# Kernel tuning notes

Measured on AMD Instinct MI355X. Metric: run time of the kernel, lower is better.

Reference implementation:

```python
import jax, jax.numpy as jnp
import numpy as np
import math

B, S, D_IN, D_OUT = 2, 2048, 2048, 2048
N_HEADS, N_KV = 32, 8
HEAD_DIM = D_OUT // N_HEADS  # 64
GROUP = N_HEADS // N_KV      # 4


def _rope_tables(seq_len, head_dim, base=10000.0):
    inv_freq = 1.0 / (base ** (jnp.arange(0, head_dim, 2, dtype=jnp.float32) / head_dim))
    angles = jnp.arange(seq_len, dtype=jnp.float32)[:, None] * inv_freq[None, :]  # [S, hd/2]
    angles = jnp.concatenate([angles, angles], axis=-1)  # [S, hd]
    return jnp.cos(angles), jnp.sin(angles)


def setup_inputs() -> dict:
    key = jax.random.key(0)
    kx, kq, kk, kv, ko = jax.random.split(key, 5)
    x = jax.random.normal(kx, (B, S, D_IN), dtype=jnp.float32)
    # causal mask: True where attention is disallowed (j > i)
    mask = jnp.triu(jnp.ones((S, S), dtype=bool), k=1)
    cos, sin = _rope_tables(S, HEAD_DIM)
    scale = 0.02
    Wq = jax.random.normal(kq, (D_IN, D_OUT), dtype=jnp.float32) * scale
    Wk = jax.random.normal(kk, (D_IN, N_KV * HEAD_DIM), dtype=jnp.float32) * scale
    Wv = jax.random.normal(kv, (D_IN, N_KV * HEAD_DIM), dtype=jnp.float32) * scale
    Wo = jax.random.normal(ko, (D_OUT, D_OUT), dtype=jnp.float32) * scale
    return {"x": x, "mask": mask, "cos": cos, "sin": sin,
            "Wq": Wq, "Wk": Wk, "Wv": Wv, "Wo": Wo}


def _apply_rope(t, cos, sin):
    # t: [B, H, S, hd]; cos/sin: [S, hd]
    hd = t.shape[-1]
    t1, t2 = t[..., : hd // 2], t[..., hd // 2:]
    rotated = jnp.concatenate([-t2, t1], axis=-1)
    return t * cos[None, None] + rotated * sin[None, None]


def reference(x, mask, cos, sin, Wq, Wk, Wv, Wo):
    b, s, _ = x.shape
    q = (x @ Wq).reshape(b, s, N_HEADS, HEAD_DIM).transpose(0, 2, 1, 3)  # [B,H,S,hd]
    k = (x @ Wk).reshape(b, s, N_KV, HEAD_DIM).transpose(0, 2, 1, 3)    # [B,G,S,hd]
    v = (x @ Wv).reshape(b, s, N_KV, HEAD_DIM).transpose(0, 2, 1, 3)
    q = _apply_rope(q, cos, sin)
    k = _apply_rope(k, cos, sin)
    # repeat_interleave KV heads to match query heads
    k = jnp.repeat(k, GROUP, axis=1)  # [B,H,S,hd]
    v = jnp.repeat(v, GROUP, axis=1)
    scores = jnp.einsum('bhqd,bhkd->bhqk', q, k)
    scores = jnp.where(mask[None, None], -1e9, scores)
    weights = jax.nn.softmax(scores / math.sqrt(HEAD_DIM), axis=-1)
    ctx = jnp.einsum('bhqk,bhkd->bhqd', weights, v)
    ctx = ctx.transpose(0, 2, 1, 3).reshape(b, s, D_OUT)
    return ctx @ Wo
```

## Files before the change

### kernel.cpp

```cpp
#include <hip/hip_runtime.h>
#include <hip/hip_bf16.h>

using bf16 = __bf16;
using bf16x8 = __attribute__((ext_vector_type(8))) __bf16;
using bf16x4 = __attribute__((ext_vector_type(4))) __bf16;
using f32x4  = __attribute__((ext_vector_type(4))) float;
using f32x16 = __attribute__((ext_vector_type(16))) float;

typedef const void __attribute__((address_space(1)))* gas_p;
typedef void __attribute__((address_space(3)))* las_p;

#define GLD16(g, l) __builtin_amdgcn_global_load_lds((gas_p)(const void*)(g), (las_p)(void*)(l), 16, 0, 0)

__device__ __forceinline__ bf16x8 lds_ld8(const void* p) {
  union { uint4 u; bf16x8 v; } c;
  c.u = *(const uint4*)p;
  return c.v;
}
__device__ __forceinline__ bf16x8 g_ld8(const bf16* p) {
  union { uint4 u; bf16x8 v; } c;
  c.u = *(const uint4*)p;
  return c.v;
}
__device__ __forceinline__ float fexp2(float x) {
  float r; asm("v_exp_f32 %0, %1" : "=v"(r) : "v"(x)); return r;
}
__device__ __forceinline__ unsigned cvtpk(float lo, float hi) {
  unsigned r; asm("v_cvt_pk_bf16_f32 %0, %1, %2" : "=v"(r) : "v"(lo), "v"(hi)); return r;
}

__global__ void k_convert(const float* __restrict__ in, bf16* __restrict__ out, int n4) {
  int i = blockIdx.x * blockDim.x + threadIdx.x;
  if (i >= n4) return;
  float4 f = ((const float4*)in)[i];
  bf16x4 o;
  o[0] = (bf16)f.x; o[1] = (bf16)f.y; o[2] = (bf16)f.z; o[3] = (bf16)f.w;
  ((bf16x4*)out)[i] = o;
}

__global__ void k_transp_all(const float* __restrict__ Wq, const float* __restrict__ Wk,
                             const float* __restrict__ Wv, const float* __restrict__ Wo,
                             bf16* __restrict__ wqkv, bf16* __restrict__ wo_t) {
  __shared__ float tile[64][65];
  const int id = blockIdx.x;
  const float* W; bf16* dst; int N, rowOff, bx, by;
  if (id < 1024)      { W = Wq; dst = wqkv; N = 2048; rowOff = 0;    bx = id & 31;          by = id >> 5; }
  else if (id < 1280) { int u = id - 1024; W = Wk; dst = wqkv; N = 512; rowOff = 2048; bx = u & 7; by = u >> 3; }
  else if (id < 1536) { int u = id - 1280; W = Wv; dst = wqkv; N = 512; rowOff = 2560; bx = u & 7; by = u >> 3; }
  else                { int u = id - 1536; W = Wo; dst = wo_t; N = 2048; rowOff = 0;   bx = u & 31; by = u >> 5; }
  const int n0 = bx * 64, k0 = by * 64;
  const int t = threadIdx.x;
#pragma unroll
  for (int i = 0; i < 16; ++i) {
    int idx = t + i * 256; int r = idx >> 6, c = idx & 63;
    tile[r][c] = W[(size_t)(k0 + r) * N + n0 + c];
  }
  __syncthreads();
#pragma unroll
  for (int i = 0; i < 16; ++i) {
    int idx = t + i * 256; int r = idx >> 6, c = idx & 63;
    dst[(size_t)(rowOff + n0 + r) * 2048 + k0 + c] = (bf16)tile[c][r];
  }
}

__device__ __forceinline__ void gemm_main(const bf16* __restrict__ A, const bf16* __restrict__ Bt,
                                          int brow, int bcol, int tid, f32x4 (&acc)[4][4],
                                          char* ldsA, char* ldsB) {
  const int lane = tid & 63;
  const int l15 = lane & 15, l4 = lane >> 4;
  const int wid = tid >> 6, wr = wid >> 1, wc = wid & 1;
  const int srow = tid >> 3;
  const int xseg = (tid & 7) ^ (srow & 7);
  const bf16* ga = A  + (size_t)(brow + srow) * 2048 + xseg * 8;
  const bf16* gb = Bt + (size_t)(bcol + srow) * 2048 + xseg * 8;
  char* la = ldsA + tid * 16;
  char* lb = ldsB + tid * 16;

  for (int k0 = 0; k0 < 2048; k0 += 64) {
    __syncthreads();
#pragma unroll
    for (int i = 0; i < 4; ++i) {
      GLD16(ga + k0 + (size_t)(32 * i) * 2048, la + i * 4096);
      GLD16(gb + k0 + (size_t)(32 * i) * 2048, lb + i * 4096);
    }
    __syncthreads();
#pragma unroll
    for (int kk = 0; kk < 2; ++kk) {
      bf16x8 af[4], bfr[4];
#pragma unroll
      for (int m = 0; m < 4; ++m) {
        const int row = wr * 64 + m * 16 + l15;
        af[m] = lds_ld8(ldsA + row * 128 + ((kk * 64 + l4 * 16) ^ ((row & 7) << 4)));
      }
#pragma unroll
      for (int n = 0; n < 4; ++n) {
        const int row = wc * 64 + n * 16 + l15;
        bfr[n] = lds_ld8(ldsB + row * 128 + ((kk * 64 + l4 * 16) ^ ((row & 7) << 4)));
      }
#pragma unroll
      for (int m = 0; m < 4; ++m)
#pragma unroll
        for (int n = 0; n < 4; ++n)
          acc[m][n] = __builtin_amdgcn_mfma_f32_16x16x32_bf16(af[m], bfr[n], acc[m][n], 0, 0, 0);
    }
  }
}

__global__ __launch_bounds__(256) void k_gemm_qkv(const bf16* __restrict__ A, const bf16* __restrict__ Bt,
    const float* __restrict__ cosT, const float* __restrict__ sinT,
    bf16* __restrict__ Qb, bf16* __restrict__ Kb, bf16* __restrict__ Vt) {
  __shared__ __align__(16) char ldsA[16384];
  __shared__ __align__(16) char ldsB[16384];
  const int tid = threadIdx.x;
  const int p = (int)blockIdx.x, r8 = p & 7, q8 = p >> 3;
  const int by = r8 * 3 + q8 % 3, bx = q8 / 3;
  const int brow = bx * 128, bcol = by * 128;
  f32x4 zero = {0.f, 0.f, 0.f, 0.f};
  f32x4 acc[4][4];
#pragma unroll
  for (int m = 0; m < 4; ++m)
#pragma unroll
    for (int n = 0; n < 4; ++n) acc[m][n] = zero;

  gemm_main(A, Bt, brow, bcol, tid, acc, ldsA, ldsB);

  const int lane = tid & 63, l15 = lane & 15, l4 = lane >> 4;
  const int wid = tid >> 6, wr = wid >> 1, wc = wid & 1;
  const int base64 = bcol + wc * 64;
  const int rbase  = brow + wr * 64;

  if (base64 < 2048) {
    const int h = base64 >> 6;
#pragma unroll
    for (int m = 0; m < 4; ++m)
#pragma unroll
      for (int r = 0; r < 4; ++r) {
        const int row = rbase + m * 16 + l4 * 4 + r;
        const int b = row >> 11, s = row & 2047;
        float o[4];
#pragma unroll
        for (int n = 0; n < 4; ++n) {
          const int d = n * 16 + l15;
          const float cv = cosT[s * 64 + d], sv = sinT[s * 64 + d];
          const float t = acc[m][n][r], pp = acc[m][n ^ 2][r];
          o[n] = (t * cv + ((n < 2) ? -pp : pp) * sv) * 0.18033688f;
        }
        bf16* dst = Qb + ((size_t)((b * 32 + h) * 2048 + s)) * 64;
#pragma unroll
        for (int n = 0; n < 4; ++n) dst[n * 16 + l15] = (bf16)o[n];
      }
  } else if (base64 < 2560) {
    const int h = (base64 - 2048) >> 6;
#pragma unroll
    for (int m = 0; m < 4; ++m)
#pragma unroll
      for (int r = 0; r < 4; ++r) {
        const int row = rbase + m * 16 + l4 * 4 + r;
        const int b = row >> 11, s = row & 2047;
        float o[4];
#pragma unroll
        for (int n = 0; n < 4; ++n) {
          const int d = n * 16 + l15;
          const float cv = cosT[s * 64 + d], sv = sinT[s * 64 + d];
          const float t = acc[m][n][r], pp = acc[m][n ^ 2][r];
          o[n] = t * cv + ((n < 2) ? -pp : pp) * sv;
        }
        bf16* dst = Kb + ((size_t)((b * 8 + h) * 2048 + s)) * 64;
#pragma unroll
        for (int n = 0; n < 4; ++n) dst[n * 16 + l15] = (bf16)o[n];
      }
  } else {
    const int h = (base64 - 2560) >> 6;
#pragma unroll
    for (int m = 0; m < 4; ++m)
#pragma unroll
      for (int r = 0; r < 4; ++r) {
        const int row = rbase + m * 16 + l4 * 4 + r;
        const int b = row >> 11, s = row & 2047;
        const int ps = (s & ~12) | ((s & 4) << 1) | ((s & 8) >> 1);
#pragma unroll
        for (int n = 0; n < 4; ++n) {
          const int d = n * 16 + l15;
          Vt[((size_t)((b * 8 + h) * 64 + d)) * 2048 + ps] = (bf16)acc[m][n][r];
        }
      }
  }
}

__global__ __launch_bounds__(256) void k_attn(const bf16* __restrict__ Qb, const bf16* __restrict__ Kb,
                                              const bf16* __restrict__ Vtp, bf16* __restrict__ ctx) {
  __shared__ __align__(16) char kvb[2][16384];
  __shared__ __align__(16) char tbuf[4][4096];
  const int tid = threadIdx.x, lane = tid & 63, w = tid >> 6;
  const int l31 = lane & 31, hi = lane >> 5;
  const int p = (int)blockIdx.x;
  const int y = (p & 7) * 8 + ((p >> 3) & 7);
  const int j = p >> 6;
  const int b = y >> 5, h = y & 31, hk = h >> 2;
  const int ntA = 2 * (15 - j) + 2;
  const int NT = 34;

  const int srow = tid >> 3, sseg = tid & 7;
  const bf16* kS = Kb  + ((size_t)((b * 8 + hk) * 2048)) * 64;
  const bf16* vS = Vtp + ((size_t)((b * 8 + hk) * 64)) * 2048;
  const int sz = (l31 & 7) << 4;
  const int wsz = (srow & 7) << 4;

  const f32x16 z16 = {0,0,0,0,0,0,0,0,0,0,0,0,0,0,0,0};
  f32x16 o[2];
  float m, lsum;
  bf16x8 bq[4];
  int c = 15 - j;
  int q0 = c * 128 + w * 32;
  int nf = (q0 + 31) >> 6;

  auto load_q = [&]() {
    const bf16* qbase = Qb + ((size_t)((b * 32 + h) * 2048 + q0 + l31)) * 64 + hi * 8;
#pragma unroll
    for (int dc = 0; dc < 4; ++dc) bq[dc] = g_ld8(qbase + dc * 16);
  };
  load_q();
  o[0] = z16; o[1] = z16; m = -3.0e38f; lsum = 0.f;

  uint4 st[4];
  auto stage_load = [&](int kv0) {
#pragma unroll
    for (int r4 = 0; r4 < 4; ++r4) {
      const int row = srow + (r4 & 1) * 32;
      const bf16* g = (r4 < 2) ? (kS + (size_t)(kv0 + row) * 64 + sseg * 8)
                               : (vS + (size_t)row * 2048 + kv0 + sseg * 8);
      st[r4] = *(const uint4*)g;
    }
  };
  auto stage_write = [&](char* buf) {
#pragma unroll
    for (int r4 = 0; r4 < 4; ++r4)
      *(uint4*)(buf + (srow + r4 * 32) * 128 + ((sseg * 16) ^ wsz)) = st[r4];
  };

  auto epilogue = [&]() {
    float ll = lsum + __shfl_xor(lsum, 32);
    const float inv = 1.0f / ll;
    char* tb = tbuf[w];
#pragma unroll
    for (int dh = 0; dh < 2; ++dh)
#pragma unroll
      for (int r = 0; r < 16; r += 2) {
        const unsigned wdv = cvtpk(o[dh][r] * inv, o[dh][r + 1] * inv);
        const int d = dh * 32 + (r & 3) + 8 * (r >> 2) + 4 * hi;
        *(unsigned*)(tb + l31 * 128 + ((d * 2) ^ sz)) = wdv;
      }
#pragma unroll
    for (int jj = 0; jj < 4; ++jj) {
      const int off = hi * 16 + jj * 32;
      uint4 val = *(const uint4*)(tb + l31 * 128 + (off ^ sz));
      *(uint4*)(ctx + ((size_t)(b * 2048 + q0 + l31)) * 2048 + h * 64 + off / 2) = val;
    }
  };

  stage_load(0);
  stage_write(kvb[0]);
  __syncthreads();

  for (int g = 0; g < NT; ++g) {
    const int kt = (g < ntA) ? g : g - ntA;
    char* cur = kvb[g & 1];
    if (g + 1 < NT) {
      const int gn = g + 1;
      const int ktn = (gn < ntA) ? gn : gn - ntA;
      stage_load(ktn * 64);
    }
    if (kt <= nf) {
      const int kv0 = kt * 64;
      f32x16 sc[2];
      __builtin_amdgcn_s_setprio(1);
#pragma unroll
      for (int kvh = 0; kvh < 2; ++kvh) {
        const int row = kvh * 32 + l31;
        bf16x8 a0 = lds_ld8(cur + row * 128 + ((hi * 16) ^ sz));
        sc[kvh] = __builtin_amdgcn_mfma_f32_32x32x16_bf16(a0, bq[0], z16, 0, 0, 0);
#pragma unroll
        for (int dc = 1; dc < 4; ++dc) {
          bf16x8 ad = lds_ld8(cur + row * 128 + ((dc * 32 + hi * 16) ^ sz));
          sc[kvh] = __builtin_amdgcn_mfma_f32_32x32x16_bf16(ad, bq[dc], sc[kvh], 0, 0, 0);
        }
      }
      __builtin_amdgcn_s_setprio(0);
      if (kt == nf) {
        const int q = q0 + l31;
#pragma unroll
        for (int kvh = 0; kvh < 2; ++kvh)
#pragma unroll
          for (int r = 0; r < 16; ++r) {
            const int kv = kv0 + kvh * 32 + (r & 3) + 8 * (r >> 2) + 4 * hi;
            if (kv > q) sc[kvh][r] = -3.0e30f;
          }
      }
      float t[16];
#pragma unroll
      for (int i = 0; i < 16; ++i) t[i] = fmaxf(sc[0][i], sc[1][i]);
#pragma unroll
      for (int stp = 8; stp >= 1; stp >>= 1)
#pragma unroll
        for (int i = 0; i < stp; ++i) t[i] = fmaxf(t[i], t[i + stp]);
      float mx = fmaxf(t[0], __shfl_xor(t[0], 32));
      if (!__all(mx <= m + 11.5f)) {
        const float mn = fmaxf(m, mx);
        const float corr = fexp2(m - mn);
        m = mn;
        lsum *= corr;
#pragma unroll
        for (int r = 0; r < 16; ++r) { o[0][r] *= corr; o[1][r] *= corr; }
      }
#pragma unroll
      for (int kvh = 0; kvh < 2; ++kvh)
#pragma unroll
        for (int r = 0; r < 16; ++r) sc[kvh][r] = fexp2(sc[kvh][r] - m);
#pragma unroll
      for (int kvh = 0; kvh < 2; ++kvh)
#pragma unroll
        for (int s = 0; s < 2; ++s) {
          union { unsigned u[4]; bf16x8 v; } f;
#pragma unroll
          for (int tt = 0; tt < 4; ++tt)
            f.u[tt] = cvtpk(sc[kvh][s * 8 + 2 * tt], sc[kvh][s * 8 + 2 * tt + 1]);
          const int cc = kvh * 2 + s;
          __builtin_amdgcn_s_setprio(1);
#pragma unroll
          for (int dh = 0; dh < 2; ++dh) {
            const int row = 64 + dh * 32 + l31;
            bf16x8 av = lds_ld8(cur + row * 128 + ((cc * 32 + hi * 16) ^ sz));
            o[dh] = __builtin_amdgcn_mfma_f32_32x32x16_bf16(av, f.v, o[dh], 0, 0, 0);
          }
          __builtin_amdgcn_s_setprio(0);
        }
      float u[16];
#pragma unroll
      for (int i = 0; i < 16; ++i) u[i] = sc[0][i] + sc[1][i];
#pragma unroll
      for (int stp = 8; stp >= 1; stp >>= 1)
#pragma unroll
        for (int i = 0; i < stp; ++i) u[i] += u[i + stp];
      lsum += u[0];
    }
    if (g + 1 < NT) stage_write(kvb[(g + 1) & 1]);
    __syncthreads();
    if (g == ntA - 1) {
      epilogue();
      c = j; q0 = c * 128 + w * 32; nf = (q0 + 31) >> 6;
      load_q();
      o[0] = z16; o[1] = z16; m = -3.0e38f; lsum = 0.f;
    }
  }
  epilogue();
}

__global__ __launch_bounds__(256) void k_gemm_out(const bf16* __restrict__ A, const bf16* __restrict__ Bt,
                                                  float* __restrict__ out) {
  __shared__ __align__(16) char ldsA[16384];
  __shared__ __align__(16) char ldsB[16384];
  const int tid = threadIdx.x;
  const int p = (int)blockIdx.x, r8 = p & 7, q8 = p >> 3;
  const int by = r8 * 2 + (q8 & 1), bx = q8 >> 1;
  const int brow = bx * 128, bcol = by * 128;
  f32x4 zero = {0.f, 0.f, 0.f, 0.f};
  f32x4 acc[4][4];
#pragma unroll
  for (int m = 0; m < 4; ++m)
#pragma unroll
    for (int n = 0; n < 4; ++n) acc[m][n] = zero;

  gemm_main(A, Bt, brow, bcol, tid, acc, ldsA, ldsB);

  const int lane = tid & 63, l15 = lane & 15, l4 = lane >> 4;
  const int wid = tid >> 6, wr = wid >> 1, wc = wid & 1;
#pragma unroll
  for (int m = 0; m < 4; ++m)
#pragma unroll
    for (int r = 0; r < 4; ++r) {
      const int row = brow + wr * 64 + m * 16 + l4 * 4 + r;
      float* dst = out + (size_t)row * 2048 + bcol + wc * 64;
#pragma unroll
      for (int n = 0; n < 4; ++n) dst[n * 16 + l15] = acc[m][n][r];
    }
}

extern "C" void kernel_launch(void* const* d_in, const int* in_sizes, int n_in,
                              void* d_out, int out_size, void* d_ws, size_t ws_size,
                              hipStream_t stream) {
  (void)in_sizes; (void)n_in; (void)out_size;
  if (ws_size < (size_t)79691776) return;
  const float* x    = (const float*)d_in[0];
  const float* cosT = (const float*)d_in[2];
  const float* sinT = (const float*)d_in[3];
  const float* Wq   = (const float*)d_in[4];
  const float* Wk   = (const float*)d_in[5];
  const float* Wv   = (const float*)d_in[6];
  const float* Wo   = (const float*)d_in[7];
  char* ws = (char*)d_ws;
  bf16* xb   = (bf16*)(ws + 0);
  bf16* wqkv = (bf16*)(ws + 16777216);
  bf16* wo_t = (bf16*)(ws + 29360128);
  bf16* Qb   = (bf16*)(ws + 37748736);
  bf16* Kb   = (bf16*)(ws + 54525952);
  bf16* Vt   = (bf16*)(ws + 58720256);
  bf16* ctxb = (bf16*)(ws + 62914560);
  float* out = (float*)d_out;

  k_convert<<<8192, 256, 0, stream>>>(x, xb, 2097152);
  k_transp_all<<<2560, 256, 0, stream>>>(Wq, Wk, Wv, Wo, wqkv, wo_t);
  k_gemm_qkv<<<768, 256, 0, stream>>>(xb, wqkv, cosT, sinT, Qb, Kb, Vt);
  k_attn<<<512, 256, 0, stream>>>(Qb, Kb, Vt, ctxb);
  k_gemm_out<<<512, 256, 0, stream>>>(ctxb, wo_t, out);
}
```

Measured before the change: 211.4 us.

## Split attention KV tiles across wave pairs and fuse preprocessing kernels

The attention kernel now handles 64-row query chunks, with each pair of waves splitting the KV tiles by parity. Partial softmax states (max, sum, output) are merged through LDS in a new merge step. The grid doubles to 1024 blocks with a launch-bounds occupancy hint, and the separate tbuf is dropped in favour of reusing the KV buffer. The x conversion and weight transpose kernels are also fused into one launch. This aims to shorten the causal tail and raise parallelism, at the cost of extra barriers and LDS merge traffic.

```diff
diff --git a/kernel.cpp b/kernel.cpp
--- a/kernel.cpp
+++ b/kernel.cpp
@@ -29,25 +29,26 @@
   unsigned r; asm("v_cvt_pk_bf16_f32 %0, %1, %2" : "=v"(r) : "v"(lo), "v"(hi)); return r;
 }
 
-__global__ void k_convert(const float* __restrict__ in, bf16* __restrict__ out, int n4) {
-  int i = blockIdx.x * blockDim.x + threadIdx.x;
-  if (i >= n4) return;
-  float4 f = ((const float4*)in)[i];
-  bf16x4 o;
-  o[0] = (bf16)f.x; o[1] = (bf16)f.y; o[2] = (bf16)f.z; o[3] = (bf16)f.w;
-  ((bf16x4*)out)[i] = o;
-}
-
-__global__ void k_transp_all(const float* __restrict__ Wq, const float* __restrict__ Wk,
-                             const float* __restrict__ Wv, const float* __restrict__ Wo,
-                             bf16* __restrict__ wqkv, bf16* __restrict__ wo_t) {
+__global__ void k_pre(const float* __restrict__ x, bf16* __restrict__ xb,
+                      const float* __restrict__ Wq, const float* __restrict__ Wk,
+                      const float* __restrict__ Wv, const float* __restrict__ Wo,
+                      bf16* __restrict__ wqkv, bf16* __restrict__ wo_t) {
+  const int id = blockIdx.x;
+  if (id < 8192) {
+    const int i = id * 256 + threadIdx.x;
+    float4 f = ((const float4*)x)[i];
+    bf16x4 o;
+    o[0] = (bf16)f.x; o[1] = (bf16)f.y; o[2] = (bf16)f.z; o[3] = (bf16)f.w;
+    ((bf16x4*)xb)[i] = o;
+    return;
+  }
   __shared__ float tile[64][65];
-  const int id = blockIdx.x;
+  const int u0 = id - 8192;
   const float* W; bf16* dst; int N, rowOff, bx, by;
-  if (id < 1024)      { W = Wq; dst = wqkv; N = 2048; rowOff = 0;    bx = id & 31;          by = id >> 5; }
-  else if (id < 1280) { int u = id - 1024; W = Wk; dst = wqkv; N = 512; rowOff = 2048; bx = u & 7; by = u >> 3; }
-  else if (id < 1536) { int u = id - 1280; W = Wv; dst = wqkv; N = 512; rowOff = 2560; bx = u & 7; by = u >> 3; }
-  else                { int u = id - 1536; W = Wo; dst = wo_t; N = 2048; rowOff = 0;   bx = u & 31; by = u >> 5; }
+  if (u0 < 1024)      { W = Wq; dst = wqkv; N = 2048; rowOff = 0;    bx = u0 & 31; by = u0 >> 5; }
+  else if (u0 < 1280) { int u = u0 - 1024; W = Wk; dst = wqkv; N = 512; rowOff = 2048; bx = u & 7; by = u >> 3; }
+  else if (u0 < 1536) { int u = u0 - 1280; W = Wv; dst = wqkv; N = 512; rowOff = 2560; bx = u & 7; by = u >> 3; }
+  else                { int u = u0 - 1536; W = Wo; dst = wo_t; N = 2048; rowOff = 0;   bx = u & 31; by = u >> 5; }
   const int n0 = bx * 64, k0 = by * 64;
   const int t = threadIdx.x;
 #pragma unroll
@@ -187,18 +188,20 @@
   }
 }
 
-__global__ __launch_bounds__(256) void k_attn(const bf16* __restrict__ Qb, const bf16* __restrict__ Kb,
-                                              const bf16* __restrict__ Vtp, bf16* __restrict__ ctx) {
+__global__ __launch_bounds__(256, 4) void k_attn(const bf16* __restrict__ Qb, const bf16* __restrict__ Kb,
+                                                 const bf16* __restrict__ Vtp, bf16* __restrict__ ctx) {
   __shared__ __align__(16) char kvb[2][16384];
-  __shared__ __align__(16) char tbuf[4][4096];
   const int tid = threadIdx.x, lane = tid & 63, w = tid >> 6;
   const int l31 = lane & 31, hi = lane >> 5;
+  const int sub = w >> 1, par = w & 1;
   const int p = (int)blockIdx.x;
   const int y = (p & 7) * 8 + ((p >> 3) & 7);
   const int j = p >> 6;
   const int b = y >> 5, h = y & 31, hk = h >> 2;
-  const int ntA = 2 * (15 - j) + 2;
-  const int NT = 34;
+  int c = 31 - j;
+  const int ntA = c + 1;
+  const int NT = 33;
+  int q0 = c * 64 + sub * 32;
 
   const int srow = tid >> 3, sseg = tid & 7;
   const bf16* kS = Kb  + ((size_t)((b * 8 + hk) * 2048)) * 64;
@@ -210,9 +213,6 @@
   f32x16 o[2];
   float m, lsum;
   bf16x8 bq[4];
-  int c = 15 - j;
-  int q0 = c * 128 + w * 32;
-  int nf = (q0 + 31) >> 6;
 
   auto load_q = [&]() {
     const bf16* qbase = Qb + ((size_t)((b * 32 + h) * 2048 + q0 + l31)) * 64 + hi * 8;
@@ -238,24 +238,54 @@
       *(uint4*)(buf + (srow + r4 * 32) * 128 + ((sseg * 16) ^ wsz)) = st[r4];
   };
 
-  auto epilogue = [&]() {
-    float ll = lsum + __shfl_xor(lsum, 32);
-    const float inv = 1.0f / ll;
-    char* tb = tbuf[w];
-#pragma unroll
-    for (int dh = 0; dh < 2; ++dh)
-#pragma unroll
-      for (int r = 0; r < 16; r += 2) {
-        const unsigned wdv = cvtpk(o[dh][r] * inv, o[dh][r + 1] * inv);
-        const int d = dh * 32 + (r & 3) + 8 * (r >> 2) + 4 * hi;
-        *(unsigned*)(tb + l31 * 128 + ((d * 2) ^ sz)) = wdv;
-      }
-#pragma unroll
-    for (int jj = 0; jj < 4; ++jj) {
-      const int off = hi * 16 + jj * 32;
-      uint4 val = *(const uint4*)(tb + l31 * 128 + (off ^ sz));
-      *(uint4*)(ctx + ((size_t)(b * 2048 + q0 + l31)) * 2048 + h * 64 + off / 2) = val;
-    }
+  auto merge_store = [&](char* fb) {
+    float* mz = (float*)fb;
+    float* lz = (float*)(fb + 512);
+    float* oz = (float*)(fb + 1024 + sub * 4096);
+    if (par == 1) {
+      mz[sub * 64 + lane] = m;
+      lz[sub * 64 + lane] = lsum;
+#pragma unroll
+      for (int r = 0; r < 16; ++r) oz[r * 64 + lane] = o[0][r];
+    }
+    __syncthreads();
+    float ca = 0.f, cb = 0.f, inv = 0.f;
+    if (par == 0) {
+      const float m2 = mz[sub * 64 + lane], l2 = lz[sub * 64 + lane];
+      const float M = fmaxf(m, m2);
+      ca = fexp2(m - M); cb = fexp2(m2 - M);
+      float ll = lsum * ca + l2 * cb;
+      ll += __shfl_xor(ll, 32);
+      inv = 1.0f / ll;
+#pragma unroll
+      for (int r = 0; r < 16; ++r) o[0][r] = o[0][r] * ca + oz[r * 64 + lane] * cb;
+    }
+    __syncthreads();
+    if (par == 1) {
+#pragma unroll
+      for (int r = 0; r < 16; ++r) oz[r * 64 + lane] = o[1][r];
+    }
+    __syncthreads();
+    if (par == 0) {
+#pragma unroll
+      for (int r = 0; r < 16; ++r) o[1][r] = o[1][r] * ca + oz[r * 64 + lane] * cb;
+      char* tb = (char*)oz;
+#pragma unroll
+      for (int dh = 0; dh < 2; ++dh)
+#pragma unroll
+        for (int r = 0; r < 16; r += 2) {
+          const unsigned wdv = cvtpk(o[dh][r] * inv, o[dh][r + 1] * inv);
+          const int d = dh * 32 + (r & 3) + 8 * (r >> 2) + 4 * hi;
+          *(unsigned*)(tb + l31 * 128 + ((d * 2) ^ sz)) = wdv;
+        }
+#pragma unroll
+      for (int jj = 0; jj < 4; ++jj) {
+        const int off = hi * 16 + jj * 32;
+        uint4 val = *(const uint4*)(tb + l31 * 128 + (off ^ sz));
+        *(uint4*)(ctx + ((size_t)(b * 2048 + q0 + l31)) * 2048 + h * 64 + off / 2) = val;
+      }
+    }
+    __syncthreads();
   };
 
   stage_load(0);
@@ -267,10 +297,9 @@
     char* cur = kvb[g & 1];
     if (g + 1 < NT) {
       const int gn = g + 1;
-      const int ktn = (gn < ntA) ? gn : gn - ntA;
-      stage_load(ktn * 64);
-    }
-    if (kt <= nf) {
+      stage_load(((gn < ntA) ? gn : gn - ntA) * 64);
+    }
+    if ((kt & 1) == par) {
       const int kv0 = kt * 64;
       f32x16 sc[2];
       __builtin_amdgcn_s_setprio(1);
@@ -286,7 +315,7 @@
         }
       }
       __builtin_amdgcn_s_setprio(0);
-      if (kt == nf) {
+      if (kt == c) {
         const int q = q0 + l31;
 #pragma unroll
         for (int kvh = 0; kvh < 2; ++kvh)
@@ -346,13 +375,13 @@
     if (g + 1 < NT) stage_write(kvb[(g + 1) & 1]);
     __syncthreads();
     if (g == ntA - 1) {
-      epilogue();
-      c = j; q0 = c * 128 + w * 32; nf = (q0 + 31) >> 6;
+      merge_store(kvb[g & 1]);
+      c = j; q0 = c * 64 + sub * 32;
       load_q();
       o[0] = z16; o[1] = z16; m = -3.0e38f; lsum = 0.f;
     }
   }
-  epilogue();
+  merge_store(kvb[(NT - 1) & 1]);
 }
 
 __global__ __launch_bounds__(256) void k_gemm_out(const bf16* __restrict__ A, const bf16* __restrict__ Bt,
@@ -407,9 +436,8 @@
   bf16* ctxb = (bf16*)(ws + 62914560);
   float* out = (float*)d_out;
 
-  k_convert<<<8192, 256, 0, stream>>>(x, xb, 2097152);
-  k_transp_all<<<2560, 256, 0, stream>>>(Wq, Wk, Wv, Wo, wqkv, wo_t);
+  k_pre<<<10752, 256, 0, stream>>>(x, xb, Wq, Wk, Wv, Wo, wqkv, wo_t);
   k_gemm_qkv<<<768, 256, 0, stream>>>(xb, wqkv, cosT, sinT, Qb, Kb, Vt);
-  k_attn<<<512, 256, 0, stream>>>(Qb, Kb, Vt, ctxb);
+  k_attn<<<1024, 256, 0, stream>>>(Qb, Kb, Vt, ctxb);
   k_gemm_out<<<512, 256, 0, stream>>>(ctxb, wo_t, out);
 }
```

After: 291.1 us. 1.38x slower.

## Defer PV MFMA to next iteration with triple-buffered KV and fuse preprocessing kernels

Applied to the files above, without the earlier changes.

The attention loop now converts probabilities to bf16 and defers the P·V MFMAs to the start of the next iteration. This lets the next tile's QK MFMAs and softmax overlap with them, and needs a third LDS KV buffer so the deferred tile stays valid. The input conversion and weight transpose kernels are merged into one launch to save a launch. The extra LDS raises shared memory use per block and may cut occupancy.

```diff
diff --git a/kernel.cpp b/kernel.cpp
--- a/kernel.cpp
+++ b/kernel.cpp
@@ -29,25 +29,26 @@
   unsigned r; asm("v_cvt_pk_bf16_f32 %0, %1, %2" : "=v"(r) : "v"(lo), "v"(hi)); return r;
 }
 
-__global__ void k_convert(const float* __restrict__ in, bf16* __restrict__ out, int n4) {
-  int i = blockIdx.x * blockDim.x + threadIdx.x;
-  if (i >= n4) return;
-  float4 f = ((const float4*)in)[i];
-  bf16x4 o;
-  o[0] = (bf16)f.x; o[1] = (bf16)f.y; o[2] = (bf16)f.z; o[3] = (bf16)f.w;
-  ((bf16x4*)out)[i] = o;
-}
-
-__global__ void k_transp_all(const float* __restrict__ Wq, const float* __restrict__ Wk,
-                             const float* __restrict__ Wv, const float* __restrict__ Wo,
-                             bf16* __restrict__ wqkv, bf16* __restrict__ wo_t) {
+__global__ void k_pre(const float* __restrict__ x, bf16* __restrict__ xb,
+                      const float* __restrict__ Wq, const float* __restrict__ Wk,
+                      const float* __restrict__ Wv, const float* __restrict__ Wo,
+                      bf16* __restrict__ wqkv, bf16* __restrict__ wo_t) {
+  const int id = blockIdx.x;
+  if (id < 8192) {
+    const int i = id * 256 + threadIdx.x;
+    float4 f = ((const float4*)x)[i];
+    bf16x4 o;
+    o[0] = (bf16)f.x; o[1] = (bf16)f.y; o[2] = (bf16)f.z; o[3] = (bf16)f.w;
+    ((bf16x4*)xb)[i] = o;
+    return;
+  }
   __shared__ float tile[64][65];
-  const int id = blockIdx.x;
+  const int u0 = id - 8192;
   const float* W; bf16* dst; int N, rowOff, bx, by;
-  if (id < 1024)      { W = Wq; dst = wqkv; N = 2048; rowOff = 0;    bx = id & 31;          by = id >> 5; }
-  else if (id < 1280) { int u = id - 1024; W = Wk; dst = wqkv; N = 512; rowOff = 2048; bx = u & 7; by = u >> 3; }
-  else if (id < 1536) { int u = id - 1280; W = Wv; dst = wqkv; N = 512; rowOff = 2560; bx = u & 7; by = u >> 3; }
-  else                { int u = id - 1536; W = Wo; dst = wo_t; N = 2048; rowOff = 0;   bx = u & 31; by = u >> 5; }
+  if (u0 < 1024)      { W = Wq; dst = wqkv; N = 2048; rowOff = 0;    bx = u0 & 31; by = u0 >> 5; }
+  else if (u0 < 1280) { int u = u0 - 1024; W = Wk; dst = wqkv; N = 512; rowOff = 2048; bx = u & 7; by = u >> 3; }
+  else if (u0 < 1536) { int u = u0 - 1280; W = Wv; dst = wqkv; N = 512; rowOff = 2560; bx = u & 7; by = u >> 3; }
+  else                { int u = u0 - 1536; W = Wo; dst = wo_t; N = 2048; rowOff = 0;   bx = u & 31; by = u >> 5; }
   const int n0 = bx * 64, k0 = by * 64;
   const int t = threadIdx.x;
 #pragma unroll
@@ -189,7 +190,7 @@
 
 __global__ __launch_bounds__(256) void k_attn(const bf16* __restrict__ Qb, const bf16* __restrict__ Kb,
                                               const bf16* __restrict__ Vtp, bf16* __restrict__ ctx) {
-  __shared__ __align__(16) char kvb[2][16384];
+  __shared__ __align__(16) char kvb[3][16384];
   __shared__ __align__(16) char tbuf[4][4096];
   const int tid = threadIdx.x, lane = tid & 63, w = tid >> 6;
   const int l31 = lane & 31, hi = lane >> 5;
@@ -197,8 +198,11 @@
   const int y = (p & 7) * 8 + ((p >> 3) & 7);
   const int j = p >> 6;
   const int b = y >> 5, h = y & 31, hk = h >> 2;
-  const int ntA = 2 * (15 - j) + 2;
+  int c = 15 - j;
+  const int ntA = 2 * c + 2;
   const int NT = 34;
+  int q0 = c * 128 + w * 32;
+  int nf = (q0 + 31) >> 6;
 
   const int srow = tid >> 3, sseg = tid & 7;
   const bf16* kS = Kb  + ((size_t)((b * 8 + hk) * 2048)) * 64;
@@ -210,9 +214,6 @@
   f32x16 o[2];
   float m, lsum;
   bf16x8 bq[4];
-  int c = 15 - j;
-  int q0 = c * 128 + w * 32;
-  int nf = (q0 + 31) >> 6;
 
   auto load_q = [&]() {
     const bf16* qbase = Qb + ((size_t)((b * 32 + h) * 2048 + q0 + l31)) * 64 + hi * 8;
@@ -238,6 +239,23 @@
       *(uint4*)(buf + (srow + r4 * 32) * 128 + ((sseg * 16) ^ wsz)) = st[r4];
   };
 
+  union PF { unsigned u[4]; bf16x8 v; };
+  PF pf[4];
+  int pend = 0, pslot = 0;
+
+  auto pv_issue = [&](char* pbuf) {
+    __builtin_amdgcn_s_setprio(1);
+#pragma unroll
+    for (int cc = 0; cc < 4; ++cc)
+#pragma unroll
+      for (int dh = 0; dh < 2; ++dh) {
+        const int row = 64 + dh * 32 + l31;
+        bf16x8 av = lds_ld8(pbuf + row * 128 + ((cc * 32 + hi * 16) ^ sz));
+        o[dh] = __builtin_amdgcn_mfma_f32_32x32x16_bf16(av, pf[cc].v, o[dh], 0, 0, 0);
+      }
+    __builtin_amdgcn_s_setprio(0);
+  };
+
   auto epilogue = [&]() {
     float ll = lsum + __shfl_xor(lsum, 32);
     const float inv = 1.0f / ll;
@@ -264,12 +282,12 @@
 
   for (int g = 0; g < NT; ++g) {
     const int kt = (g < ntA) ? g : g - ntA;
-    char* cur = kvb[g & 1];
+    char* cur = kvb[g % 3];
     if (g + 1 < NT) {
       const int gn = g + 1;
-      const int ktn = (gn < ntA) ? gn : gn - ntA;
-      stage_load(ktn * 64);
-    }
+      stage_load(((gn < ntA) ? gn : gn - ntA) * 64);
+    }
+    if (pend) { pv_issue(kvb[pslot]); pend = 0; }
     if (kt <= nf) {
       const int kv0 = kt * 64;
       f32x16 sc[2];
@@ -319,21 +337,11 @@
 #pragma unroll
       for (int kvh = 0; kvh < 2; ++kvh)
 #pragma unroll
-        for (int s = 0; s < 2; ++s) {
-          union { unsigned u[4]; bf16x8 v; } f;
+        for (int s = 0; s < 2; ++s)
 #pragma unroll
           for (int tt = 0; tt < 4; ++tt)
-            f.u[tt] = cvtpk(sc[kvh][s * 8 + 2 * tt], sc[kvh][s * 8 + 2 * tt + 1]);
-          const int cc = kvh * 2 + s;
-          __builtin_amdgcn_s_setprio(1);
-#pragma unroll
-          for (int dh = 0; dh < 2; ++dh) {
-            const int row = 64 + dh * 32 + l31;
-            bf16x8 av = lds_ld8(cur + row * 128 + ((cc * 32 + hi * 16) ^ sz));
-            o[dh] = __builtin_amdgcn_mfma_f32_32x32x16_bf16(av, f.v, o[dh], 0, 0, 0);
-          }
-          __builtin_amdgcn_s_setprio(0);
-        }
+            pf[kvh * 2 + s].u[tt] = cvtpk(sc[kvh][s * 8 + 2 * tt], sc[kvh][s * 8 + 2 * tt + 1]);
+      pend = 1; pslot = g % 3;
       float u[16];
 #pragma unroll
       for (int i = 0; i < 16; ++i) u[i] = sc[0][i] + sc[1][i];
@@ -343,15 +351,17 @@
         for (int i = 0; i < stp; ++i) u[i] += u[i + stp];
       lsum += u[0];
     }
-    if (g + 1 < NT) stage_write(kvb[(g + 1) & 1]);
+    if (g + 1 < NT) stage_write(kvb[(g + 1) % 3]);
     __syncthreads();
     if (g == ntA - 1) {
+      if (pend) { pv_issue(kvb[pslot]); pend = 0; }
       epilogue();
       c = j; q0 = c * 128 + w * 32; nf = (q0 + 31) >> 6;
       load_q();
       o[0] = z16; o[1] = z16; m = -3.0e38f; lsum = 0.f;
     }
   }
+  if (pend) { pv_issue(kvb[pslot]); pend = 0; }
   epilogue();
 }
 
@@ -407,8 +417,7 @@
   bf16* ctxb = (bf16*)(ws + 62914560);
   float* out = (float*)d_out;
 
-  k_convert<<<8192, 256, 0, stream>>>(x, xb, 2097152);
-  k_transp_all<<<2560, 256, 0, stream>>>(Wq, Wk, Wv, Wo, wqkv, wo_t);
+  k_pre<<<10752, 256, 0, stream>>>(x, xb, Wq, Wk, Wv, Wo, wqkv, wo_t);
   k_gemm_qkv<<<768, 256, 0, stream>>>(xb, wqkv, cosT, sinT, Qb, Kb, Vt);
   k_attn<<<512, 256, 0, stream>>>(Qb, Kb, Vt, ctxb);
   k_gemm_out<<<512, 256, 0, stream>>>(ctxb, wo_t, out);
```

New measurement: 217.6 us. 3.0% more time.
